# Kernel optimization log

Hardware: AMD Instinct MI355X
Metric: run time of the kernel (lower is better)

## Reference

```python
import jax, jax.numpy as jnp
import numpy as np

B, L, H = 64, 1024, 512  # batch, seq_len, hidden_units; encoder feature = 2H


def setup_inputs() -> dict:
    key = jax.random.key(0)
    k1, k2, k3, k4, k5 = jax.random.split(key, 5)
    scale = 1.0 / np.sqrt(3 * H)
    return {
        "hidden": jax.random.normal(k1, (B, H), dtype=jnp.float32),
        "encoder_outputs": jax.random.normal(k2, (B, L, 2 * H), dtype=jnp.float32),
        "W_attn": jax.random.normal(k3, (3 * H, H), dtype=jnp.float32) * scale,
        "b_attn": jax.random.normal(k4, (H,), dtype=jnp.float32) * scale,
        "W_v": jax.random.normal(k5, (H, 1), dtype=jnp.float32) * (1.0 / np.sqrt(H)),
    }


def reference(hidden, encoder_outputs, W_attn, b_attn, W_v):
    # hidden: [B, H] broadcast along seq -> [B, L, H] (torch repeat+transpose)
    b, l, e = encoder_outputs.shape
    h_rep = jnp.broadcast_to(hidden[:, None, :], (b, l, hidden.shape[-1]))
    cat = jnp.concatenate([h_rep, encoder_outputs], axis=-1)     # [B, L, 3H]
    energy = jax.nn.relu(cat @ W_attn + b_attn)                  # [B, L, H]
    attention = (energy @ W_v)[..., 0]                           # [B, L]
    weights = jax.nn.softmax(attention, axis=1)                  # [B, L]
    # bmm([B,1,L], [B,L,E]) -> [B,1,E]
    context = jnp.einsum("bl,ble->be", weights, encoder_outputs)[:, None, :]
    return context
```

## Files before the change

kernel.cpp:

```cpp
#include <hip/hip_runtime.h>
#include <hip/hip_bf16.h>

typedef __attribute__((ext_vector_type(8))) __bf16 bf16x8;
typedef __attribute__((ext_vector_type(4))) __bf16 bf16x4;
typedef __attribute__((ext_vector_type(4))) float f32x4;


#define KPAD 40
#define NKT 32

__global__ void qk(const float* __restrict__ hidden, const float* __restrict__ W_attn,
                   const float* __restrict__ b_attn, float* __restrict__ q) {
    int idx = blockIdx.x * 256 + threadIdx.x;
    int b = idx >> 9;
    int h = idx & 511;
    const float* hv = hidden + b * 512;
    float acc = b_attn[h];
#pragma unroll 8
    for (int k = 0; k < 512; ++k)
        acc = fmaf(hv[k], W_attn[(size_t)k * 512 + h], acc);
    q[idx] = acc;
}

__global__ void btk(const float* __restrict__ W_attn, __bf16* __restrict__ Bt) {
    int idx = blockIdx.x * 256 + threadIdx.x;
    int n = idx >> 10;
    int k = idx & 1023;
    Bt[idx] = (__bf16)W_attn[(size_t)(512 + k) * 512 + n];
}

__global__ __launch_bounds__(256, 4) void gemm_logits3(
    const float* __restrict__ A, const __bf16* __restrict__ Bt,
    const float* __restrict__ q, const float* __restrict__ Wv,
    float* __restrict__ part)
{
    __shared__ __bf16 As[2][128 * KPAD];
    __shared__ __bf16 Bs[2][128 * KPAD];
    float* red = (float*)&Bs[0][0];

    const int bid = blockIdx.x;
    const int swz = (bid & 7) * 256 + (bid >> 3);
    const int mt = swz >> 2;
    const int nt = swz & 3;

    const int t = threadIdx.x;
    const int lane = t & 63;
    const int wid = t >> 6;
    const int wm = wid >> 1;
    const int wn = wid & 1;

    const int ar = t >> 3;
    const int ac = (t & 7) * 4;
    const float* Ag = A + (size_t)(mt * 128 + ar) * 1024 + ac;
    const int br = t >> 2;
    const int bc = (t & 3) * 8;
    const __bf16* Bg = Bt + (size_t)(nt * 128 + br) * 1024 + bc;

    f32x4 acc[4][4];
#pragma unroll
    for (int m = 0; m < 4; ++m)
#pragma unroll
        for (int n = 0; n < 4; ++n) acc[m][n] = (f32x4)0.0f;

    float4 av[4];
    bf16x8 bv[2];

#define LOADS(K0)                                                              \
    {                                                                          \
        _Pragma("unroll") for (int i = 0; i < 4; ++i)                          \
            av[i] = *(const float4*)(Ag + (size_t)i * 32768 + (K0));           \
        _Pragma("unroll") for (int i = 0; i < 2; ++i)                          \
            bv[i] = *(const bf16x8*)(Bg + (size_t)i * 65536 + (K0));           \
    }

#define WRITES(BUF)                                                            \
    {                                                                          \
        _Pragma("unroll") for (int i = 0; i < 4; ++i) {                        \
            bf16x4 w;                                                          \
            w[0] = (__bf16)av[i].x; w[1] = (__bf16)av[i].y;                    \
            w[2] = (__bf16)av[i].z; w[3] = (__bf16)av[i].w;                    \
            *(bf16x4*)&As[BUF][(ar + i * 32) * KPAD + ac] = w;                 \
        }                                                                      \
        _Pragma("unroll") for (int i = 0; i < 2; ++i)                          \
            *(bf16x8*)&Bs[BUF][(br + i * 64) * KPAD + bc] = bv[i];             \
    }

    LOADS(0)
    WRITES(0)
    __syncthreads();

    const int rsel = lane & 15;
    const int kb = (lane >> 4) * 8;

    for (int kt = 0; kt < NKT; ++kt) {
        const int cur = kt & 1;
        if (kt + 1 < NKT) LOADS((kt + 1) * 32)

        bf16x8 af[4], bg[4];
#pragma unroll
        for (int m = 0; m < 4; ++m)
            af[m] = *(const bf16x8*)&As[cur][(wm * 64 + m * 16 + rsel) * KPAD + kb];
#pragma unroll
        for (int n = 0; n < 4; ++n)
            bg[n] = *(const bf16x8*)&Bs[cur][(wn * 64 + n * 16 + rsel) * KPAD + kb];
#pragma unroll
        for (int m = 0; m < 4; ++m)
#pragma unroll
            for (int n = 0; n < 4; ++n)
                acc[m][n] = __builtin_amdgcn_mfma_f32_16x16x32_bf16(
                    af[m], bg[n], acc[m][n], 0, 0, 0);

        if (kt + 1 < NKT) {
            WRITES(cur ^ 1)
            __syncthreads();
        }
    }
#undef LOADS
#undef WRITES

    __syncthreads();

    const float* qb = q + (mt >> 3) * 512;
    float qv[4], wvv[4];
#pragma unroll
    for (int n = 0; n < 4; ++n) {
        int gc = nt * 128 + wn * 64 + n * 16 + rsel;
        qv[n] = qb[gc];
        wvv[n] = Wv[gc];
    }

#pragma unroll
    for (int m = 0; m < 4; ++m) {
#pragma unroll
        for (int j = 0; j < 4; ++j) {
            float s = 0.f;
#pragma unroll
            for (int n = 0; n < 4; ++n) {
                float e = acc[m][n][j] + qv[n];
                s += (e > 0.f ? e : 0.f) * wvv[n];
            }
            s += __shfl_xor(s, 1);
            s += __shfl_xor(s, 2);
            s += __shfl_xor(s, 4);
            s += __shfl_xor(s, 8);
            if (rsel == 0) {
                int r = wm * 64 + m * 16 + (lane >> 4) * 4 + j;
                red[r * 2 + wn] = s;
            }
        }
    }
    __syncthreads();
    if (t < 128)
        part[(size_t)nt * 65536 + (size_t)mt * 128 + t] = red[t * 2] + red[t * 2 + 1];
}

__global__ void softmax_k(const float* __restrict__ part, float* __restrict__ w) {
    __shared__ float smx[4];
    __shared__ float ssum[4];
    int b = blockIdx.x;
    int t = threadIdx.x;
    int lane = t & 63, wid = t >> 6;
    float v[4];
    float mx = -3.0e38f;
#pragma unroll
    for (int i = 0; i < 4; ++i) {
        int o = b * 1024 + t + i * 256;
        float s = part[o] + part[65536 + o] + part[131072 + o] + part[196608 + o];
        v[i] = s;
        mx = fmaxf(mx, s);
    }
#pragma unroll
    for (int off = 32; off >= 1; off >>= 1) mx = fmaxf(mx, __shfl_xor(mx, off));
    if (lane == 0) smx[wid] = mx;
    __syncthreads();
    mx = fmaxf(fmaxf(smx[0], smx[1]), fmaxf(smx[2], smx[3]));
    float e[4];
    float sum = 0.f;
#pragma unroll
    for (int i = 0; i < 4; ++i) { e[i] = __expf(v[i] - mx); sum += e[i]; }
#pragma unroll
    for (int off = 32; off >= 1; off >>= 1) sum += __shfl_xor(sum, off);
    if (lane == 0) ssum[wid] = sum;
    __syncthreads();
    float inv = 1.f / (ssum[0] + ssum[1] + ssum[2] + ssum[3]);
#pragma unroll
    for (int i = 0; i < 4; ++i) w[b * 1024 + t + i * 256] = e[i] * inv;
}

__global__ void ctx_partial(const float* __restrict__ enc, const float* __restrict__ w,
                            float* __restrict__ ctxp) {
    int blk = blockIdx.x;
    int b = blk >> 3;
    int lc = blk & 7;
    int t = threadIdx.x;
    __shared__ float wl[128];
    if (t < 128) wl[t] = w[b * 1024 + lc * 128 + t];
    __syncthreads();
    float4 acc = {0.f, 0.f, 0.f, 0.f};
    const float* base = enc + ((size_t)(b * 1024 + lc * 128)) * 1024 + t * 4;
    for (int l = 0; l < 128; ++l) {
        float4 v = *(const float4*)(base + (size_t)l * 1024);
        float s = wl[l];
        acc.x += s * v.x; acc.y += s * v.y; acc.z += s * v.z; acc.w += s * v.w;
    }
    *(float4*)(ctxp + (size_t)(lc * 64 + b) * 1024 + t * 4) = acc;
}

__global__ void ctx_sum(const float* __restrict__ ctxp, float* __restrict__ out) {
    int idx = blockIdx.x * 256 + threadIdx.x;
    float4 a = {0.f, 0.f, 0.f, 0.f};
#pragma unroll
    for (int lc = 0; lc < 8; ++lc) {
        float4 v = *(const float4*)(ctxp + (size_t)lc * 65536 + (size_t)idx * 4);
        a.x += v.x; a.y += v.y; a.z += v.z; a.w += v.w;
    }
    *(float4*)(out + (size_t)idx * 4) = a;
}

extern "C" void kernel_launch(void* const* d_in, const int* in_sizes, int n_in,
                              void* d_out, int out_size, void* d_ws, size_t ws_size,
                              hipStream_t stream) {
    const float* hidden = (const float*)d_in[0];
    const float* enc    = (const float*)d_in[1];
    const float* W_attn = (const float*)d_in[2];
    const float* b_attn = (const float*)d_in[3];
    const float* W_v    = (const float*)d_in[4];
    float* out = (float*)d_out;

    char* ws = (char*)d_ws;
    float*  q    = (float*)(ws + 0);
    __bf16* Bt   = (__bf16*)(ws + 131072);
    float*  part = (float*)(ws + 1179648);
    float*  wts  = (float*)(ws + 2228224);
    float*  ctxp = (float*)(ws + 2490368);

    qk<<<128, 256, 0, stream>>>(hidden, W_attn, b_attn, q);
    btk<<<2048, 256, 0, stream>>>(W_attn, Bt);
    gemm_logits3<<<2048, 256, 0, stream>>>(enc, Bt, q, W_v, part);
    softmax_k<<<64, 256, 0, stream>>>(part, wts);
    ctx_partial<<<512, 256, 0, stream>>>(enc, wts, ctxp);
    ctx_sum<<<64, 256, 0, stream>>>(ctxp, out);
}
```

Measured before the change: 188.2 us.

## Stage GEMM tiles via direct global-to-LDS loads with XOR-swizzled layouts

The logits GEMM now uses global_load_lds to copy fp32 encoder tiles and a pre-swizzled bf16 weight image straight into shared memory, which removes the register round-trip and the separate LDS write step. The bf16 conversion of the A operand moves to fragment-read time. XOR swizzles replace the padded layout to avoid bank conflicts, and the weight prep kernel writes the swizzled image directly. In exchange, the A tile is stored as fp32, so LDS use doubles for it and occupancy drops from 4 to 3 blocks; each tile is also converted redundantly by every wave that reads it, and the loop relies on a single barrier per step.

```diff
diff --git a/kernel.cpp b/kernel.cpp
--- a/kernel.cpp
+++ b/kernel.cpp
@@ -2,11 +2,9 @@
 #include <hip/hip_bf16.h>
 
 typedef __attribute__((ext_vector_type(8))) __bf16 bf16x8;
-typedef __attribute__((ext_vector_type(4))) __bf16 bf16x4;
 typedef __attribute__((ext_vector_type(4))) float f32x4;
 
 
-#define KPAD 40
 #define NKT 32
 
 __global__ void qk(const float* __restrict__ hidden, const float* __restrict__ W_attn,
@@ -22,21 +20,33 @@
     q[idx] = acc;
 }
 
-__global__ void btk(const float* __restrict__ W_attn, __bf16* __restrict__ Bt) {
+__global__ void btk_img2(const float* __restrict__ W_attn, __bf16* __restrict__ Bimg) {
     int idx = blockIdx.x * 256 + threadIdx.x;
-    int n = idx >> 10;
-    int k = idx & 1023;
-    Bt[idx] = (__bf16)W_attn[(size_t)(512 + k) * 512 + n];
-}
-
-__global__ __launch_bounds__(256, 4) void gemm_logits3(
-    const float* __restrict__ A, const __bf16* __restrict__ Bt,
+    int e    = idx & 7;
+    int slot = (idx >> 3) & 3;
+    int row  = (idx >> 5) & 127;
+    int kt   = (idx >> 12) & 31;
+    int nt   = idx >> 17;
+    int c = slot ^ (row & 3) ^ ((row >> 2) & 1);
+    int k = kt * 32 + c * 8 + e;
+    int n = nt * 128 + row;
+    Bimg[idx] = (__bf16)W_attn[(size_t)(512 + k) * 512 + n];
+}
+
+__device__ inline void gl_lds16(const void* g, void* l) {
+    __builtin_amdgcn_global_load_lds(
+        (const __attribute__((address_space(1))) void*)g,
+        (__attribute__((address_space(3))) void*)l, 16, 0, 0);
+}
+
+__global__ __launch_bounds__(256, 3) void gemm_logits4(
+    const float* __restrict__ A, const __bf16* __restrict__ Bimg,
     const float* __restrict__ q, const float* __restrict__ Wv,
     float* __restrict__ part)
 {
-    __shared__ __bf16 As[2][128 * KPAD];
-    __shared__ __bf16 Bs[2][128 * KPAD];
-    float* red = (float*)&Bs[0][0];
+    __shared__ float  As[2][4096];
+    __shared__ __bf16 Bs[2][4096];
+    float* red = (float*)&As[0][0];
 
     const int bid = blockIdx.x;
     const int swz = (bid & 7) * 256 + (bid >> 3);
@@ -49,12 +59,9 @@
     const int wm = wid >> 1;
     const int wn = wid & 1;
 
-    const int ar = t >> 3;
-    const int ac = (t & 7) * 4;
-    const float* Ag = A + (size_t)(mt * 128 + ar) * 1024 + ac;
-    const int br = t >> 2;
-    const int bc = (t & 3) * 8;
-    const __bf16* Bg = Bt + (size_t)(nt * 128 + br) * 1024 + bc;
+    const float* Asrc = A + (size_t)(mt * 128 + wid * 32 + (lane >> 3)) * 1024
+                          + (((lane & 7) ^ (lane >> 3)) << 2);
+    const __bf16* Bsrc = Bimg + (size_t)nt * 32 * 4096 + (wid * 2) * 512 + lane * 8;
 
     f32x4 acc[4][4];
 #pragma unroll
@@ -62,47 +69,48 @@
 #pragma unroll
         for (int n = 0; n < 4; ++n) acc[m][n] = (f32x4)0.0f;
 
-    float4 av[4];
-    bf16x8 bv[2];
-
-#define LOADS(K0)                                                              \
+#define STAGE(KT, BUF)                                                         \
     {                                                                          \
         _Pragma("unroll") for (int i = 0; i < 4; ++i)                          \
-            av[i] = *(const float4*)(Ag + (size_t)i * 32768 + (K0));           \
+            gl_lds16(Asrc + (size_t)i * 8192 + (KT) * 32,                      \
+                     &As[BUF][(wid * 4 + i) * 256]);                           \
         _Pragma("unroll") for (int i = 0; i < 2; ++i)                          \
-            bv[i] = *(const bf16x8*)(Bg + (size_t)i * 65536 + (K0));           \
-    }
-
-#define WRITES(BUF)                                                            \
-    {                                                                          \
-        _Pragma("unroll") for (int i = 0; i < 4; ++i) {                        \
-            bf16x4 w;                                                          \
-            w[0] = (__bf16)av[i].x; w[1] = (__bf16)av[i].y;                    \
-            w[2] = (__bf16)av[i].z; w[3] = (__bf16)av[i].w;                    \
-            *(bf16x4*)&As[BUF][(ar + i * 32) * KPAD + ac] = w;                 \
-        }                                                                      \
-        _Pragma("unroll") for (int i = 0; i < 2; ++i)                          \
-            *(bf16x8*)&Bs[BUF][(br + i * 64) * KPAD + bc] = bv[i];             \
-    }
-
-    LOADS(0)
-    WRITES(0)
+            gl_lds16(Bsrc + (size_t)(KT) * 4096 + i * 512,                     \
+                     &Bs[BUF][(wid * 2 + i) * 512]);                           \
+    }
+
+    STAGE(0, 0)
     __syncthreads();
 
     const int rsel = lane & 15;
-    const int kb = (lane >> 4) * 8;
+    const int qq = lane >> 4;
+    const int h = rsel & 7;
+    const int s0 = (2 * qq) ^ h;
+    const int s1 = (2 * qq + 1) ^ h;
+    const int bslot = qq ^ (rsel & 3) ^ ((rsel >> 2) & 1);
 
     for (int kt = 0; kt < NKT; ++kt) {
         const int cur = kt & 1;
-        if (kt + 1 < NKT) LOADS((kt + 1) * 32)
+        if (kt + 1 < NKT) STAGE(kt + 1, cur ^ 1)
 
         bf16x8 af[4], bg[4];
 #pragma unroll
-        for (int m = 0; m < 4; ++m)
-            af[m] = *(const bf16x8*)&As[cur][(wm * 64 + m * 16 + rsel) * KPAD + kb];
-#pragma unroll
-        for (int n = 0; n < 4; ++n)
-            bg[n] = *(const bf16x8*)&Bs[cur][(wn * 64 + n * 16 + rsel) * KPAD + kb];
+        for (int m = 0; m < 4; ++m) {
+            const int row = wm * 64 + m * 16 + rsel;
+            float4 f0 = *(const float4*)&As[cur][row * 32 + s0 * 4];
+            float4 f1 = *(const float4*)&As[cur][row * 32 + s1 * 4];
+            bf16x8 v;
+            v[0] = (__bf16)f0.x; v[1] = (__bf16)f0.y;
+            v[2] = (__bf16)f0.z; v[3] = (__bf16)f0.w;
+            v[4] = (__bf16)f1.x; v[5] = (__bf16)f1.y;
+            v[6] = (__bf16)f1.z; v[7] = (__bf16)f1.w;
+            af[m] = v;
+        }
+#pragma unroll
+        for (int n = 0; n < 4; ++n) {
+            const int row = wn * 64 + n * 16 + rsel;
+            bg[n] = *(const bf16x8*)&Bs[cur][row * 32 + bslot * 8];
+        }
 #pragma unroll
         for (int m = 0; m < 4; ++m)
 #pragma unroll
@@ -110,15 +118,9 @@
                 acc[m][n] = __builtin_amdgcn_mfma_f32_16x16x32_bf16(
                     af[m], bg[n], acc[m][n], 0, 0, 0);
 
-        if (kt + 1 < NKT) {
-            WRITES(cur ^ 1)
-            __syncthreads();
-        }
-    }
-#undef LOADS
-#undef WRITES
-
-    __syncthreads();
+        __syncthreads();
+    }
+#undef STAGE
 
     const float* qb = q + (mt >> 3) * 512;
     float qv[4], wvv[4];
@@ -229,14 +231,14 @@
 
     char* ws = (char*)d_ws;
     float*  q    = (float*)(ws + 0);
-    __bf16* Bt   = (__bf16*)(ws + 131072);
+    __bf16* Bimg = (__bf16*)(ws + 131072);
     float*  part = (float*)(ws + 1179648);
     float*  wts  = (float*)(ws + 2228224);
     float*  ctxp = (float*)(ws + 2490368);
 
     qk<<<128, 256, 0, stream>>>(hidden, W_attn, b_attn, q);
-    btk<<<2048, 256, 0, stream>>>(W_attn, Bt);
-    gemm_logits3<<<2048, 256, 0, stream>>>(enc, Bt, q, W_v, part);
+    btk_img2<<<2048, 256, 0, stream>>>(W_attn, Bimg);
+    gemm_logits4<<<2048, 256, 0, stream>>>(enc, Bimg, q, W_v, part);
     softmax_k<<<64, 256, 0, stream>>>(part, wts);
     ctx_partial<<<512, 256, 0, stream>>>(enc, wts, ctxp);
     ctx_sum<<<64, 256, 0, stream>>>(ctxp, out);
```

Measured after the change: 216.2 us. +14.9%, slower.

## Restructure logits GEMM with XOR-swizzled LDS and two-deep register prefetch

Applied to the files above, without the earlier changes.

Rewrites the main MFMA GEMM kernel. A and B tiles now share one XOR-swizzled LDS array instead of padded rows, and each thread loads contiguous 16-element row segments. Global loads are prefetched two k-tiles ahead in double register buffers, the loop is manually unrolled by two with a custom barrier, and s_setprio is raised around the MFMA burst. The goal is to hide global load latency and remove LDS bank conflicts, at the cost of more registers, which is why the occupancy hint drops from 4 to 3 blocks.

```diff
diff --git a/kernel.cpp b/kernel.cpp
--- a/kernel.cpp
+++ b/kernel.cpp
@@ -2,12 +2,8 @@
 #include <hip/hip_bf16.h>
 
 typedef __attribute__((ext_vector_type(8))) __bf16 bf16x8;
-typedef __attribute__((ext_vector_type(4))) __bf16 bf16x4;
 typedef __attribute__((ext_vector_type(4))) float f32x4;
 
-
-#define KPAD 40
-#define NKT 32
 
 __global__ void qk(const float* __restrict__ hidden, const float* __restrict__ W_attn,
                    const float* __restrict__ b_attn, float* __restrict__ q) {
@@ -29,14 +25,13 @@
     Bt[idx] = (__bf16)W_attn[(size_t)(512 + k) * 512 + n];
 }
 
-__global__ __launch_bounds__(256, 4) void gemm_logits3(
+__global__ __launch_bounds__(256, 3) void gemm_logits5(
     const float* __restrict__ A, const __bf16* __restrict__ Bt,
     const float* __restrict__ q, const float* __restrict__ Wv,
     float* __restrict__ part)
 {
-    __shared__ __bf16 As[2][128 * KPAD];
-    __shared__ __bf16 Bs[2][128 * KPAD];
-    float* red = (float*)&Bs[0][0];
+    __shared__ __bf16 Ls[2][128][64];
+    __shared__ float red[128][2];
 
     const int bid = blockIdx.x;
     const int swz = (bid & 7) * 256 + (bid >> 3);
@@ -49,12 +44,13 @@
     const int wm = wid >> 1;
     const int wn = wid & 1;
 
-    const int ar = t >> 3;
-    const int ac = (t & 7) * 4;
-    const float* Ag = A + (size_t)(mt * 128 + ar) * 1024 + ac;
-    const int br = t >> 2;
-    const int bc = (t & 3) * 8;
-    const __bf16* Bg = Bt + (size_t)(nt * 128 + br) * 1024 + bc;
+    const int srow = t >> 1;
+    const int shalf = t & 1;
+    const float* Ag = A + (size_t)(mt * 128 + srow) * 1024 + shalf * 16;
+    const __bf16* Bg = Bt + (size_t)(nt * 128 + srow) * 1024 + shalf * 16;
+    const int rx = srow & 7;
+    const int wa0 = (shalf * 2) ^ rx,     wa1 = (shalf * 2 + 1) ^ rx;
+    const int wb0 = (4 + shalf * 2) ^ rx, wb1 = (4 + shalf * 2 + 1) ^ rx;
 
     f32x4 acc[4][4];
 #pragma unroll
@@ -62,63 +58,90 @@
 #pragma unroll
         for (int n = 0; n < 4; ++n) acc[m][n] = (f32x4)0.0f;
 
-    float4 av[4];
-    bf16x8 bv[2];
-
-#define LOADS(K0)                                                              \
+    float4 aS[2][4];
+    bf16x8 bS[2][2];
+
+#define LOADS(P, KT)                                                           \
     {                                                                          \
-        _Pragma("unroll") for (int i = 0; i < 4; ++i)                          \
-            av[i] = *(const float4*)(Ag + (size_t)i * 32768 + (K0));           \
-        _Pragma("unroll") for (int i = 0; i < 2; ++i)                          \
-            bv[i] = *(const bf16x8*)(Bg + (size_t)i * 65536 + (K0));           \
-    }
-
-#define WRITES(BUF)                                                            \
+        const float* ap = Ag + (size_t)(KT) * 32;                              \
+        aS[P][0] = *(const float4*)(ap);                                       \
+        aS[P][1] = *(const float4*)(ap + 4);                                   \
+        aS[P][2] = *(const float4*)(ap + 8);                                   \
+        aS[P][3] = *(const float4*)(ap + 12);                                  \
+        const __bf16* bp = Bg + (size_t)(KT) * 32;                             \
+        bS[P][0] = *(const bf16x8*)(bp);                                       \
+        bS[P][1] = *(const bf16x8*)(bp + 8);                                   \
+    }
+
+#define WRITES(P, BUF)                                                         \
     {                                                                          \
-        _Pragma("unroll") for (int i = 0; i < 4; ++i) {                        \
-            bf16x4 w;                                                          \
-            w[0] = (__bf16)av[i].x; w[1] = (__bf16)av[i].y;                    \
-            w[2] = (__bf16)av[i].z; w[3] = (__bf16)av[i].w;                    \
-            *(bf16x4*)&As[BUF][(ar + i * 32) * KPAD + ac] = w;                 \
+        bf16x8 v0, v1;                                                         \
+        v0[0] = (__bf16)aS[P][0].x; v0[1] = (__bf16)aS[P][0].y;                \
+        v0[2] = (__bf16)aS[P][0].z; v0[3] = (__bf16)aS[P][0].w;                \
+        v0[4] = (__bf16)aS[P][1].x; v0[5] = (__bf16)aS[P][1].y;                \
+        v0[6] = (__bf16)aS[P][1].z; v0[7] = (__bf16)aS[P][1].w;                \
+        v1[0] = (__bf16)aS[P][2].x; v1[1] = (__bf16)aS[P][2].y;                \
+        v1[2] = (__bf16)aS[P][2].z; v1[3] = (__bf16)aS[P][2].w;                \
+        v1[4] = (__bf16)aS[P][3].x; v1[5] = (__bf16)aS[P][3].y;                \
+        v1[6] = (__bf16)aS[P][3].z; v1[7] = (__bf16)aS[P][3].w;                \
+        *(bf16x8*)&Ls[BUF][srow][wa0 * 8] = v0;                                \
+        *(bf16x8*)&Ls[BUF][srow][wa1 * 8] = v1;                                \
+        *(bf16x8*)&Ls[BUF][srow][wb0 * 8] = bS[P][0];                          \
+        *(bf16x8*)&Ls[BUF][srow][wb1 * 8] = bS[P][1];                          \
+    }
+
+#define BARRIER()                                                              \
+    do {                                                                       \
+        asm volatile("s_waitcnt lgkmcnt(0)" ::: "memory");                     \
+        __builtin_amdgcn_s_barrier();                                          \
+        __builtin_amdgcn_sched_barrier(0);                                     \
+    } while (0)
+
+    const int rsel = lane & 15;
+    const int qq = lane >> 4;
+
+#define FRAGS_MFMA(CUR)                                                        \
+    {                                                                          \
+        bf16x8 af[4];                                                          \
+        _Pragma("unroll") for (int m = 0; m < 4; ++m) {                        \
+            const int row = wm * 64 + m * 16 + rsel;                           \
+            af[m] = *(const bf16x8*)&Ls[CUR][row][(qq ^ (row & 7)) * 8];       \
         }                                                                      \
-        _Pragma("unroll") for (int i = 0; i < 2; ++i)                          \
-            *(bf16x8*)&Bs[BUF][(br + i * 64) * KPAD + bc] = bv[i];             \
-    }
-
-    LOADS(0)
-    WRITES(0)
-    __syncthreads();
-
-    const int rsel = lane & 15;
-    const int kb = (lane >> 4) * 8;
-
-    for (int kt = 0; kt < NKT; ++kt) {
-        const int cur = kt & 1;
-        if (kt + 1 < NKT) LOADS((kt + 1) * 32)
-
-        bf16x8 af[4], bg[4];
-#pragma unroll
-        for (int m = 0; m < 4; ++m)
-            af[m] = *(const bf16x8*)&As[cur][(wm * 64 + m * 16 + rsel) * KPAD + kb];
-#pragma unroll
-        for (int n = 0; n < 4; ++n)
-            bg[n] = *(const bf16x8*)&Bs[cur][(wn * 64 + n * 16 + rsel) * KPAD + kb];
-#pragma unroll
-        for (int m = 0; m < 4; ++m)
-#pragma unroll
-            for (int n = 0; n < 4; ++n)
-                acc[m][n] = __builtin_amdgcn_mfma_f32_16x16x32_bf16(
-                    af[m], bg[n], acc[m][n], 0, 0, 0);
-
-        if (kt + 1 < NKT) {
-            WRITES(cur ^ 1)
-            __syncthreads();
-        }
-    }
+        __builtin_amdgcn_s_setprio(1);                                         \
+        _Pragma("unroll") for (int n = 0; n < 4; ++n) {                        \
+            const int row = wn * 64 + n * 16 + rsel;                           \
+            bf16x8 bg = *(const bf16x8*)&Ls[CUR][row][((4 + qq) ^ (row & 7)) * 8]; \
+            _Pragma("unroll") for (int m = 0; m < 4; ++m)                      \
+                acc[m][n] = __builtin_amdgcn_mfma_f32_16x16x32_bf16(           \
+                    af[m], bg, acc[m][n], 0, 0, 0);                            \
+        }                                                                      \
+        __builtin_amdgcn_s_setprio(0);                                         \
+    }
+
+    LOADS(0, 0)
+    LOADS(1, 1)
+    WRITES(0, 0)
+    BARRIER();
+
+    for (int ki = 0; ki < 15; ++ki) {
+        const int kt = ki * 2;
+        LOADS(0, kt + 2)
+        FRAGS_MFMA(0)
+        WRITES(1, 1)
+        BARRIER();
+        LOADS(1, kt + 3)
+        FRAGS_MFMA(1)
+        WRITES(0, 0)
+        BARRIER();
+    }
+    FRAGS_MFMA(0)
+    WRITES(1, 1)
+    BARRIER();
+    FRAGS_MFMA(1)
+
 #undef LOADS
 #undef WRITES
-
-    __syncthreads();
+#undef FRAGS_MFMA
 
     const float* qb = q + (mt >> 3) * 512;
     float qv[4], wvv[4];
@@ -145,13 +168,13 @@
             s += __shfl_xor(s, 8);
             if (rsel == 0) {
                 int r = wm * 64 + m * 16 + (lane >> 4) * 4 + j;
-                red[r * 2 + wn] = s;
+                red[r][wn] = s;
             }
         }
     }
     __syncthreads();
     if (t < 128)
-        part[(size_t)nt * 65536 + (size_t)mt * 128 + t] = red[t * 2] + red[t * 2 + 1];
+        part[(size_t)nt * 65536 + (size_t)mt * 128 + t] = red[t][0] + red[t][1];
 }
 
 __global__ void softmax_k(const float* __restrict__ part, float* __restrict__ w) {
@@ -236,7 +259,7 @@
 
     qk<<<128, 256, 0, stream>>>(hidden, W_attn, b_attn, q);
     btk<<<2048, 256, 0, stream>>>(W_attn, Bt);
-    gemm_logits3<<<2048, 256, 0, stream>>>(enc, Bt, q, W_v, part);
+    gemm_logits5<<<2048, 256, 0, stream>>>(enc, Bt, q, W_v, part);
     softmax_k<<<64, 256, 0, stream>>>(part, wts);
     ctx_partial<<<512, 256, 0, stream>>>(enc, wts, ctxp);
     ctx_sum<<<64, 256, 0, stream>>>(ctxp, out);
```

Result: slower. 206.5 us (+9.7%).

## Enlarge logits GEMM tile to 256x256 with 512 threads and XOR-swizzled LDS

Applied to the files above, without the earlier changes.

The logits GEMM now uses a 256x256 output tile with 8 waves of 512 threads, where it used 128x128 with 4 waves. This halves the N-splits, so the encoder rows are read twice from global memory instead of four times, and the partial-logit buffer shrinks to two slices. The padded LDS layout is replaced by an XOR-swizzled 64-element row layout to avoid bank conflicts, and s_setprio wraps the MFMA block. Each wave now holds twice as many accumulators, which raises register pressure and lowers occupancy.

```diff
diff --git a/kernel.cpp b/kernel.cpp
--- a/kernel.cpp
+++ b/kernel.cpp
@@ -2,11 +2,9 @@
 #include <hip/hip_bf16.h>
 
 typedef __attribute__((ext_vector_type(8))) __bf16 bf16x8;
-typedef __attribute__((ext_vector_type(4))) __bf16 bf16x4;
 typedef __attribute__((ext_vector_type(4))) float f32x4;
 
 
-#define KPAD 40
 #define NKT 32
 
 __global__ void qk(const float* __restrict__ hidden, const float* __restrict__ W_attn,
@@ -29,86 +27,102 @@
     Bt[idx] = (__bf16)W_attn[(size_t)(512 + k) * 512 + n];
 }
 
-__global__ __launch_bounds__(256, 4) void gemm_logits3(
+__global__ __launch_bounds__(512, 2) void gemm_logits6(
     const float* __restrict__ A, const __bf16* __restrict__ Bt,
     const float* __restrict__ q, const float* __restrict__ Wv,
     float* __restrict__ part)
 {
-    __shared__ __bf16 As[2][128 * KPAD];
-    __shared__ __bf16 Bs[2][128 * KPAD];
-    float* red = (float*)&Bs[0][0];
+    __shared__ __bf16 Als[2][128][64];
+    __shared__ __bf16 Bls[2][128][64];
+    float* red = (float*)&Als[0][0][0];
 
     const int bid = blockIdx.x;
-    const int swz = (bid & 7) * 256 + (bid >> 3);
-    const int mt = swz >> 2;
-    const int nt = swz & 3;
+    const int swz = (bid & 7) * 64 + (bid >> 3);
+    const int mt = swz >> 1;
+    const int nt = swz & 1;
 
     const int t = threadIdx.x;
     const int lane = t & 63;
     const int wid = t >> 6;
-    const int wm = wid >> 1;
-    const int wn = wid & 1;
-
-    const int ar = t >> 3;
-    const int ac = (t & 7) * 4;
-    const float* Ag = A + (size_t)(mt * 128 + ar) * 1024 + ac;
-    const int br = t >> 2;
-    const int bc = (t & 3) * 8;
-    const __bf16* Bg = Bt + (size_t)(nt * 128 + br) * 1024 + bc;
-
-    f32x4 acc[4][4];
-#pragma unroll
-    for (int m = 0; m < 4; ++m)
+    const int wm = wid >> 2;
+    const int wn = wid & 3;
+
+    const int srow = t >> 1;
+    const int kh = t & 1;
+    const float*  Ag = A  + (size_t)(mt * 256 + srow) * 1024 + kh * 16;
+    const __bf16* Bg = Bt + (size_t)(nt * 256 + srow) * 1024 + kh * 16;
+    const int slrow = srow >> 1;
+    const int sl7 = slrow & 7;
+    const int ws0 = ((srow & 1) * 4 + kh * 2) ^ sl7;
+    const int ws1 = ((srow & 1) * 4 + kh * 2 + 1) ^ sl7;
+
+    f32x4 acc[8][4];
+#pragma unroll
+    for (int m = 0; m < 8; ++m)
 #pragma unroll
         for (int n = 0; n < 4; ++n) acc[m][n] = (f32x4)0.0f;
 
     float4 av[4];
     bf16x8 bv[2];
 
-#define LOADS(K0)                                                              \
+#define LOADS(KT)                                                              \
     {                                                                          \
-        _Pragma("unroll") for (int i = 0; i < 4; ++i)                          \
-            av[i] = *(const float4*)(Ag + (size_t)i * 32768 + (K0));           \
-        _Pragma("unroll") for (int i = 0; i < 2; ++i)                          \
-            bv[i] = *(const bf16x8*)(Bg + (size_t)i * 65536 + (K0));           \
+        const float* ap = Ag + (size_t)(KT) * 32;                              \
+        av[0] = *(const float4*)(ap);                                          \
+        av[1] = *(const float4*)(ap + 4);                                      \
+        av[2] = *(const float4*)(ap + 8);                                      \
+        av[3] = *(const float4*)(ap + 12);                                     \
+        const __bf16* bp = Bg + (size_t)(KT) * 32;                             \
+        bv[0] = *(const bf16x8*)(bp);                                          \
+        bv[1] = *(const bf16x8*)(bp + 8);                                      \
     }
 
 #define WRITES(BUF)                                                            \
     {                                                                          \
-        _Pragma("unroll") for (int i = 0; i < 4; ++i) {                        \
-            bf16x4 w;                                                          \
-            w[0] = (__bf16)av[i].x; w[1] = (__bf16)av[i].y;                    \
-            w[2] = (__bf16)av[i].z; w[3] = (__bf16)av[i].w;                    \
-            *(bf16x4*)&As[BUF][(ar + i * 32) * KPAD + ac] = w;                 \
-        }                                                                      \
-        _Pragma("unroll") for (int i = 0; i < 2; ++i)                          \
-            *(bf16x8*)&Bs[BUF][(br + i * 64) * KPAD + bc] = bv[i];             \
-    }
+        bf16x8 v0, v1;                                                         \
+        v0[0] = (__bf16)av[0].x; v0[1] = (__bf16)av[0].y;                      \
+        v0[2] = (__bf16)av[0].z; v0[3] = (__bf16)av[0].w;                      \
+        v0[4] = (__bf16)av[1].x; v0[5] = (__bf16)av[1].y;                      \
+        v0[6] = (__bf16)av[1].z; v0[7] = (__bf16)av[1].w;                      \
+        v1[0] = (__bf16)av[2].x; v1[1] = (__bf16)av[2].y;                      \
+        v1[2] = (__bf16)av[2].z; v1[3] = (__bf16)av[2].w;                      \
+        v1[4] = (__bf16)av[3].x; v1[5] = (__bf16)av[3].y;                      \
+        v1[6] = (__bf16)av[3].z; v1[7] = (__bf16)av[3].w;                      \
+        *(bf16x8*)&Als[BUF][slrow][ws0 * 8] = v0;                              \
+        *(bf16x8*)&Als[BUF][slrow][ws1 * 8] = v1;                              \
+        *(bf16x8*)&Bls[BUF][slrow][ws0 * 8] = bv[0];                           \
+        *(bf16x8*)&Bls[BUF][slrow][ws1 * 8] = bv[1];                           \
+    }
+
+    const int rsel = lane & 15;
+    const int qq = lane >> 4;
+    const int pa = (((rsel & 1) * 4 + qq) ^ (rsel >> 1)) * 8;
+    const int rhalf = rsel >> 1;
 
     LOADS(0)
     WRITES(0)
     __syncthreads();
 
-    const int rsel = lane & 15;
-    const int kb = (lane >> 4) * 8;
-
     for (int kt = 0; kt < NKT; ++kt) {
         const int cur = kt & 1;
-        if (kt + 1 < NKT) LOADS((kt + 1) * 32)
-
-        bf16x8 af[4], bg[4];
-#pragma unroll
-        for (int m = 0; m < 4; ++m)
-            af[m] = *(const bf16x8*)&As[cur][(wm * 64 + m * 16 + rsel) * KPAD + kb];
+        if (kt + 1 < NKT) LOADS(kt + 1)
+
+        bf16x8 af[8], bg[4];
+#pragma unroll
+        for (int m = 0; m < 8; ++m)
+            af[m] = *(const bf16x8*)&Als[cur][wm * 64 + m * 8 + rhalf][pa];
 #pragma unroll
         for (int n = 0; n < 4; ++n)
-            bg[n] = *(const bf16x8*)&Bs[cur][(wn * 64 + n * 16 + rsel) * KPAD + kb];
-#pragma unroll
-        for (int m = 0; m < 4; ++m)
+            bg[n] = *(const bf16x8*)&Bls[cur][wn * 32 + n * 8 + rhalf][pa];
+
+        __builtin_amdgcn_s_setprio(1);
+#pragma unroll
+        for (int m = 0; m < 8; ++m)
 #pragma unroll
             for (int n = 0; n < 4; ++n)
                 acc[m][n] = __builtin_amdgcn_mfma_f32_16x16x32_bf16(
                     af[m], bg[n], acc[m][n], 0, 0, 0);
+        __builtin_amdgcn_s_setprio(0);
 
         if (kt + 1 < NKT) {
             WRITES(cur ^ 1)
@@ -120,17 +134,17 @@
 
     __syncthreads();
 
-    const float* qb = q + (mt >> 3) * 512;
+    const float* qb = q + (mt >> 2) * 512;
     float qv[4], wvv[4];
 #pragma unroll
     for (int n = 0; n < 4; ++n) {
-        int gc = nt * 128 + wn * 64 + n * 16 + rsel;
+        int gc = nt * 256 + wn * 64 + n * 16 + rsel;
         qv[n] = qb[gc];
         wvv[n] = Wv[gc];
     }
 
 #pragma unroll
-    for (int m = 0; m < 4; ++m) {
+    for (int m = 0; m < 8; ++m) {
 #pragma unroll
         for (int j = 0; j < 4; ++j) {
             float s = 0.f;
@@ -144,14 +158,15 @@
             s += __shfl_xor(s, 4);
             s += __shfl_xor(s, 8);
             if (rsel == 0) {
-                int r = wm * 64 + m * 16 + (lane >> 4) * 4 + j;
-                red[r * 2 + wn] = s;
+                int r = wm * 128 + m * 16 + (lane >> 4) * 4 + j;
+                red[r * 4 + wn] = s;
             }
         }
     }
     __syncthreads();
-    if (t < 128)
-        part[(size_t)nt * 65536 + (size_t)mt * 128 + t] = red[t * 2] + red[t * 2 + 1];
+    if (t < 256)
+        part[(size_t)nt * 65536 + (size_t)mt * 256 + t] =
+            red[t * 4] + red[t * 4 + 1] + red[t * 4 + 2] + red[t * 4 + 3];
 }
 
 __global__ void softmax_k(const float* __restrict__ part, float* __restrict__ w) {
@@ -165,7 +180,7 @@
 #pragma unroll
     for (int i = 0; i < 4; ++i) {
         int o = b * 1024 + t + i * 256;
-        float s = part[o] + part[65536 + o] + part[131072 + o] + part[196608 + o];
+        float s = part[o] + part[65536 + o];
         v[i] = s;
         mx = fmaxf(mx, s);
     }
@@ -231,12 +246,12 @@
     float*  q    = (float*)(ws + 0);
     __bf16* Bt   = (__bf16*)(ws + 131072);
     float*  part = (float*)(ws + 1179648);
-    float*  wts  = (float*)(ws + 2228224);
-    float*  ctxp = (float*)(ws + 2490368);
+    float*  wts  = (float*)(ws + 1703936);
+    float*  ctxp = (float*)(ws + 1966080);
 
     qk<<<128, 256, 0, stream>>>(hidden, W_attn, b_attn, q);
     btk<<<2048, 256, 0, stream>>>(W_attn, Bt);
-    gemm_logits3<<<2048, 256, 0, stream>>>(enc, Bt, q, W_v, part);
+    gemm_logits6<<<512, 512, 0, stream>>>(enc, Bt, q, W_v, part);
     softmax_k<<<64, 256, 0, stream>>>(part, wts);
     ctx_partial<<<512, 256, 0, stream>>>(enc, wts, ctxp);
     ctx_sum<<<64, 256, 0, stream>>>(ctxp, out);
```

New measurement: 185.6 us. About the same (-1.4%).
